# Kernel tuning notes

Measured on AMD Instinct MI355X. Metric: run time of the kernel, lower is better.

The kernel has to match this reference:

```python
import jax, jax.numpy as jnp
import numpy as np

B = 2_000_000
OVERLAP_WEIGHT = 0.5
EPS = 1e-6


def setup_inputs() -> dict:
    key = jax.random.key(0)
    k1, k2 = jax.random.split(key)
    preds = jax.random.normal(k1, (B, 10), dtype=jnp.float32)
    targets = jax.random.normal(k2, (B, 10), dtype=jnp.float32)
    return {"preds": preds, "targets": targets}


def _quat_to_rot(q):
    # q: (B,4) in xyzw order, assumed normalized. Returns (B,3,3),
    # matching the (transposed-convention) matrix in the torch source.
    x, y, z, w = q[:, 0], q[:, 1], q[:, 2], q[:, 3]
    r = jnp.stack([
        1 - 2 * y * y - 2 * z * z, 2 * x * y + 2 * z * w, 2 * x * z - 2 * y * w,
        2 * x * y - 2 * z * w, 1 - 2 * x * x - 2 * z * z, 2 * y * z + 2 * x * w,
        2 * x * z + 2 * y * w, 2 * y * z - 2 * x * w, 1 - 2 * x * x - 2 * y * y,
    ], axis=-1)
    return r.reshape(-1, 3, 3)


def _overlaps(pred_params, gt_params):
    pred_c, pred_d, pred_q = pred_params[:, :3], pred_params[:, 3:6], pred_params[:, 6:]
    gt_c, gt_d, gt_q = gt_params[:, :3], gt_params[:, 3:6], gt_params[:, 6:]
    pred_q = pred_q / jnp.linalg.norm(pred_q, axis=-1, keepdims=True)
    gt_q = gt_q / jnp.linalg.norm(gt_q, axis=-1, keepdims=True)
    pred_rot = _quat_to_rot(pred_q)  # (B,3,3)
    gt_rot = _quat_to_rot(gt_q)      # (B,3,3)
    # trace(pred_rot.T @ gt_rot) = sum of elementwise products
    rot_align = jnp.clip(jnp.sum(pred_rot * gt_rot, axis=(1, 2)) / 3.0, 0.0, 1.0)
    pred_ext = jnp.abs(jnp.einsum('bij,bj->bi', pred_rot, pred_d / 2))
    gt_ext = jnp.abs(jnp.einsum('bij,bj->bi', gt_rot, gt_d / 2))
    center_diff = jnp.abs(pred_c - gt_c)
    overlap_per_axis = jnp.maximum(jnp.minimum(pred_ext, gt_ext) * 2 - center_diff, 0.0) \
        / (pred_ext + gt_ext + EPS)
    overlap = jnp.prod(overlap_per_axis, axis=-1) * rot_align
    return jnp.clip(overlap, 0.0, 1.0)


def _smooth_l1(preds, targets):
    d = preds - targets
    ad = jnp.abs(d)
    return jnp.mean(jnp.where(ad < 1.0, 0.5 * d * d, ad - 0.5))


def reference(preds, targets):
    param_loss = _smooth_l1(preds, targets)
    overlap = _overlaps(preds, targets)
    return param_loss + OVERLAP_WEIGHT * (1.0 - jnp.mean(overlap))
```

## Files before the change

kernel.cpp:

```cpp
#include <hip/hip_runtime.h>


#define B_ROWS 2000000
#define THREADS 256
#define CHUNK_ROWS 256
#define F4_SIDE 640
#define N_CHUNKS 7813
#define GRID 1024
constexpr float OVERLAP_WEIGHT = 0.5f;
constexpr float EPS_F = 1e-6f;
constexpr int TOTAL_F4 = 5000000;

__device__ __forceinline__ void gload_lds16(const float4* g, float4* l) {
    __builtin_amdgcn_global_load_lds(
        (const __attribute__((address_space(1))) void*)g,
        (__attribute__((address_space(3))) void*)l, 16, 0, 0);
}

__device__ __forceinline__ void quat_to_rot(float x, float y, float z, float w,
                                            float R[9]) {
    R[0] = 1.f - 2.f*y*y - 2.f*z*z;
    R[1] = 2.f*x*y + 2.f*z*w;
    R[2] = 2.f*x*z - 2.f*y*w;
    R[3] = 2.f*x*y - 2.f*z*w;
    R[4] = 1.f - 2.f*x*x - 2.f*z*z;
    R[5] = 2.f*y*z + 2.f*x*w;
    R[6] = 2.f*x*z + 2.f*y*w;
    R[7] = 2.f*y*z - 2.f*x*w;
    R[8] = 1.f - 2.f*x*x - 2.f*y*y;
}

__global__ __launch_bounds__(THREADS) void hybrid_loss_main(
    const float4* __restrict__ preds4, const float4* __restrict__ targets4,
    float* __restrict__ acc)
{
    __shared__ __align__(16) float4 lds[2][2][F4_SIDE];

    const int tid  = threadIdx.x;
    const int wave = tid >> 6;
    const int lane = tid & 63;

    float psum = 0.f, osum = 0.f;

    auto stage = [&](int buf, int c) {
        const int gb = c * F4_SIDE;
        for (int r = wave; r < 10; r += 4) {
            int idx = gb + r * 64 + lane;
            if (idx >= TOTAL_F4) idx = TOTAL_F4 - 1;
            gload_lds16(preds4   + idx, &lds[buf][0][r * 64]);
            gload_lds16(targets4 + idx, &lds[buf][1][r * 64]);
        }
    };

    int c = blockIdx.x;
    int cur = 0;
    stage(0, c);
    __syncthreads();

    while (true) {
        const int cn = c + GRID;
        const bool more = (cn < N_CHUNKS);
        if (more) stage(cur ^ 1, cn);

        if (c * CHUNK_ROWS + tid < B_ROWS) {
            float p[10], t[10];
            const float2* lp = reinterpret_cast<const float2*>(
                reinterpret_cast<const float*>(&lds[cur][0][0]) + tid * 10);
            const float2* lt = reinterpret_cast<const float2*>(
                reinterpret_cast<const float*>(&lds[cur][1][0]) + tid * 10);
            #pragma unroll
            for (int i = 0; i < 5; ++i) {
                float2 a = lp[i]; p[2*i] = a.x; p[2*i+1] = a.y;
                float2 b = lt[i]; t[2*i] = b.x; t[2*i+1] = b.y;
            }

            #pragma unroll
            for (int i = 0; i < 10; ++i) {
                float d  = p[i] - t[i];
                float ad = fabsf(d);
                psum += (ad < 1.f) ? 0.5f * d * d : ad - 0.5f;
            }

            float pqn = sqrtf(p[6]*p[6] + p[7]*p[7] + p[8]*p[8] + p[9]*p[9]);
            float tqn = sqrtf(t[6]*t[6] + t[7]*t[7] + t[8]*t[8] + t[9]*t[9]);
            float pri = 1.f / pqn, tri = 1.f / tqn;
            float PR[9], TR[9];
            quat_to_rot(p[6]*pri, p[7]*pri, p[8]*pri, p[9]*pri, PR);
            quat_to_rot(t[6]*tri, t[7]*tri, t[8]*tri, t[9]*tri, TR);

            float ra = 0.f;
            #pragma unroll
            for (int i = 0; i < 9; ++i) ra += PR[i] * TR[i];
            ra = fminf(fmaxf(ra * (1.f/3.f), 0.f), 1.f);

            float ov = ra;
            #pragma unroll
            for (int i = 0; i < 3; ++i) {
                float pe = fabsf(PR[3*i+0]*(p[3]*0.5f) + PR[3*i+1]*(p[4]*0.5f) + PR[3*i+2]*(p[5]*0.5f));
                float te = fabsf(TR[3*i+0]*(t[3]*0.5f) + TR[3*i+1]*(t[4]*0.5f) + TR[3*i+2]*(t[5]*0.5f));
                float cd = fabsf(p[i] - t[i]);
                float ax = fmaxf(fminf(pe, te) * 2.f - cd, 0.f) / (pe + te + EPS_F);
                ov *= ax;
            }
            ov = fminf(fmaxf(ov, 0.f), 1.f);
            osum += ov;
        }

        __syncthreads();
        if (!more) break;
        c = cn;
        cur ^= 1;
    }

    #pragma unroll
    for (int off = 32; off > 0; off >>= 1) {
        psum += __shfl_down(psum, off);
        osum += __shfl_down(osum, off);
    }
    float* red = reinterpret_cast<float*>(&lds[0][0][0]);
    if (lane == 0) { red[wave] = psum; red[4 + wave] = osum; }
    __syncthreads();
    if (tid == 0) {
        float P = red[0] + red[1] + red[2] + red[3];
        float O = red[4] + red[5] + red[6] + red[7];
        atomicAdd(&acc[0], P);
        atomicAdd(&acc[1], O);
    }
}

__global__ void hybrid_loss_finalize(const float* __restrict__ acc,
                                     float* __restrict__ out) {
    out[0] = acc[0] * (1.f / (10.f * (float)B_ROWS))
           + OVERLAP_WEIGHT * (1.f - acc[1] * (1.f / (float)B_ROWS));
}

extern "C" void kernel_launch(void* const* d_in, const int* in_sizes, int n_in,
                              void* d_out, int out_size, void* d_ws, size_t ws_size,
                              hipStream_t stream) {
    const float4* preds4   = (const float4*)d_in[0];
    const float4* targets4 = (const float4*)d_in[1];
    float* out = (float*)d_out;
    float* acc = (float*)d_ws;

    hipMemsetAsync(acc, 0, 2 * sizeof(float), stream);

    hybrid_loss_main<<<GRID, THREADS, 0, stream>>>(preds4, targets4, acc);
    hybrid_loss_finalize<<<1, 1, 0, stream>>>(acc, out);
}
```

Measured before the change: 191.2 us.

## Halve block size, split preds/targets loads per wave, unroll double-buffer loop

```diff
diff --git a/kernel.cpp b/kernel.cpp
--- a/kernel.cpp
+++ b/kernel.cpp
@@ -2,14 +2,13 @@
 
 
 #define B_ROWS 2000000
-#define THREADS 256
-#define CHUNK_ROWS 256
-#define F4_SIDE 640
-#define N_CHUNKS 7813
-#define GRID 1024
+#define THREADS 128
+#define CHUNK_ROWS 128
+#define F4_SIDE 320
+#define N_CHUNKS 15625
+#define GRID 2048
 constexpr float OVERLAP_WEIGHT = 0.5f;
 constexpr float EPS_F = 1e-6f;
-constexpr int TOTAL_F4 = 5000000;
 
 __device__ __forceinline__ void gload_lds16(const float4* g, float4* l) {
     __builtin_amdgcn_global_load_lds(
@@ -30,11 +29,12 @@
     R[8] = 1.f - 2.f*x*x - 2.f*y*y;
 }
 
-__global__ __launch_bounds__(THREADS) void hybrid_loss_main(
+__global__ __launch_bounds__(THREADS, 4) void hybrid_loss_main(
     const float4* __restrict__ preds4, const float4* __restrict__ targets4,
     float* __restrict__ acc)
 {
-    __shared__ __align__(16) float4 lds[2][2][F4_SIDE];
+    __shared__ __align__(16) float4 P0[F4_SIDE], T0[F4_SIDE];
+    __shared__ __align__(16) float4 P1[F4_SIDE], T1[F4_SIDE];
 
     const int tid  = threadIdx.x;
     const int wave = tid >> 6;
@@ -42,74 +42,80 @@
 
     float psum = 0.f, osum = 0.f;
 
-    auto stage = [&](int buf, int c) {
-        const int gb = c * F4_SIDE;
-        for (int r = wave; r < 10; r += 4) {
-            int idx = gb + r * 64 + lane;
-            if (idx >= TOTAL_F4) idx = TOTAL_F4 - 1;
-            gload_lds16(preds4   + idx, &lds[buf][0][r * 64]);
-            gload_lds16(targets4 + idx, &lds[buf][1][r * 64]);
+    auto stage = [&](float4* LP, float4* LT, int c) {
+        const int gb = c * F4_SIDE + lane;
+        if (wave == 0) {
+            #pragma unroll
+            for (int r = 0; r < 5; ++r)
+                gload_lds16(preds4 + gb + r * 64, LP + r * 64);
+        } else {
+            #pragma unroll
+            for (int r = 0; r < 5; ++r)
+                gload_lds16(targets4 + gb + r * 64, LT + r * 64);
         }
     };
 
-    int c = blockIdx.x;
-    int cur = 0;
-    stage(0, c);
-    __syncthreads();
-
-    while (true) {
-        const int cn = c + GRID;
-        const bool more = (cn < N_CHUNKS);
-        if (more) stage(cur ^ 1, cn);
-
-        if (c * CHUNK_ROWS + tid < B_ROWS) {
-            float p[10], t[10];
-            const float2* lp = reinterpret_cast<const float2*>(
-                reinterpret_cast<const float*>(&lds[cur][0][0]) + tid * 10);
-            const float2* lt = reinterpret_cast<const float2*>(
-                reinterpret_cast<const float*>(&lds[cur][1][0]) + tid * 10);
-            #pragma unroll
-            for (int i = 0; i < 5; ++i) {
-                float2 a = lp[i]; p[2*i] = a.x; p[2*i+1] = a.y;
-                float2 b = lt[i]; t[2*i] = b.x; t[2*i+1] = b.y;
-            }
-
-            #pragma unroll
-            for (int i = 0; i < 10; ++i) {
-                float d  = p[i] - t[i];
-                float ad = fabsf(d);
-                psum += (ad < 1.f) ? 0.5f * d * d : ad - 0.5f;
-            }
-
-            float pqn = sqrtf(p[6]*p[6] + p[7]*p[7] + p[8]*p[8] + p[9]*p[9]);
-            float tqn = sqrtf(t[6]*t[6] + t[7]*t[7] + t[8]*t[8] + t[9]*t[9]);
-            float pri = 1.f / pqn, tri = 1.f / tqn;
-            float PR[9], TR[9];
-            quat_to_rot(p[6]*pri, p[7]*pri, p[8]*pri, p[9]*pri, PR);
-            quat_to_rot(t[6]*tri, t[7]*tri, t[8]*tri, t[9]*tri, TR);
-
-            float ra = 0.f;
-            #pragma unroll
-            for (int i = 0; i < 9; ++i) ra += PR[i] * TR[i];
-            ra = fminf(fmaxf(ra * (1.f/3.f), 0.f), 1.f);
-
-            float ov = ra;
-            #pragma unroll
-            for (int i = 0; i < 3; ++i) {
-                float pe = fabsf(PR[3*i+0]*(p[3]*0.5f) + PR[3*i+1]*(p[4]*0.5f) + PR[3*i+2]*(p[5]*0.5f));
-                float te = fabsf(TR[3*i+0]*(t[3]*0.5f) + TR[3*i+1]*(t[4]*0.5f) + TR[3*i+2]*(t[5]*0.5f));
-                float cd = fabsf(p[i] - t[i]);
-                float ax = fmaxf(fminf(pe, te) * 2.f - cd, 0.f) / (pe + te + EPS_F);
-                ov *= ax;
-            }
-            ov = fminf(fmaxf(ov, 0.f), 1.f);
-            osum += ov;
+    auto compute = [&](const float4* LP, const float4* LT) {
+        float p[10], t[10];
+        const float2* lp = reinterpret_cast<const float2*>(
+            reinterpret_cast<const float*>(LP) + tid * 10);
+        const float2* lt = reinterpret_cast<const float2*>(
+            reinterpret_cast<const float*>(LT) + tid * 10);
+        #pragma unroll
+        for (int i = 0; i < 5; ++i) {
+            float2 a = lp[i]; p[2*i] = a.x; p[2*i+1] = a.y;
+            float2 b = lt[i]; t[2*i] = b.x; t[2*i+1] = b.y;
         }
 
+        #pragma unroll
+        for (int i = 0; i < 10; ++i) {
+            float d  = p[i] - t[i];
+            float ad = fabsf(d);
+            psum += (ad < 1.f) ? 0.5f * d * d : ad - 0.5f;
+        }
+
+        float pqn = sqrtf(p[6]*p[6] + p[7]*p[7] + p[8]*p[8] + p[9]*p[9]);
+        float tqn = sqrtf(t[6]*t[6] + t[7]*t[7] + t[8]*t[8] + t[9]*t[9]);
+        float pri = 1.f / pqn, tri = 1.f / tqn;
+        float PR[9], TR[9];
+        quat_to_rot(p[6]*pri, p[7]*pri, p[8]*pri, p[9]*pri, PR);
+        quat_to_rot(t[6]*tri, t[7]*tri, t[8]*tri, t[9]*tri, TR);
+
+        float ra = 0.f;
+        #pragma unroll
+        for (int i = 0; i < 9; ++i) ra += PR[i] * TR[i];
+        ra = fminf(fmaxf(ra * (1.f/3.f), 0.f), 1.f);
+
+        float ov = ra;
+        #pragma unroll
+        for (int i = 0; i < 3; ++i) {
+            float pe = fabsf(PR[3*i+0]*(p[3]*0.5f) + PR[3*i+1]*(p[4]*0.5f) + PR[3*i+2]*(p[5]*0.5f));
+            float te = fabsf(TR[3*i+0]*(t[3]*0.5f) + TR[3*i+1]*(t[4]*0.5f) + TR[3*i+2]*(t[5]*0.5f));
+            float cd = fabsf(p[i] - t[i]);
+            float ax = fmaxf(fminf(pe, te) * 2.f - cd, 0.f) / (pe + te + EPS_F);
+            ov *= ax;
+        }
+        ov = fminf(fmaxf(ov, 0.f), 1.f);
+        osum += ov;
+    };
+
+    int c0 = blockIdx.x;
+    stage(P0, T0, c0);
+    __syncthreads();
+    int c1 = c0 + GRID;
+
+    for (;;) {
+        if (c1 < N_CHUNKS) stage(P1, T1, c1);
+        compute(P0, T0);
         __syncthreads();
-        if (!more) break;
-        c = cn;
-        cur ^= 1;
+        if (c1 >= N_CHUNKS) break;
+        c0 = c1 + GRID;
+
+        if (c0 < N_CHUNKS) stage(P0, T0, c0);
+        compute(P1, T1);
+        __syncthreads();
+        if (c0 >= N_CHUNKS) break;
+        c1 = c0 + GRID;
     }
 
     #pragma unroll
@@ -117,14 +123,12 @@
         psum += __shfl_down(psum, off);
         osum += __shfl_down(osum, off);
     }
-    float* red = reinterpret_cast<float*>(&lds[0][0][0]);
-    if (lane == 0) { red[wave] = psum; red[4 + wave] = osum; }
+    float* red = reinterpret_cast<float*>(P0);
+    if (lane == 0) { red[wave] = psum; red[2 + wave] = osum; }
     __syncthreads();
     if (tid == 0) {
-        float P = red[0] + red[1] + red[2] + red[3];
-        float O = red[4] + red[5] + red[6] + red[7];
-        atomicAdd(&acc[0], P);
-        atomicAdd(&acc[1], O);
+        atomicAdd(&acc[0], red[0] + red[1]);
+        atomicAdd(&acc[1], red[2] + red[3]);
     }
 }
 
```

After: 213.1 us. +11.4%, slower.

## Replace direct global-to-LDS loads with register-staged double buffering

Applied to the files above, without the earlier changes.

```diff
diff --git a/kernel.cpp b/kernel.cpp
--- a/kernel.cpp
+++ b/kernel.cpp
@@ -10,12 +10,6 @@
 constexpr float OVERLAP_WEIGHT = 0.5f;
 constexpr float EPS_F = 1e-6f;
 constexpr int TOTAL_F4 = 5000000;
-
-__device__ __forceinline__ void gload_lds16(const float4* g, float4* l) {
-    __builtin_amdgcn_global_load_lds(
-        (const __attribute__((address_space(1))) void*)g,
-        (__attribute__((address_space(3))) void*)l, 16, 0, 0);
-}
 
 __device__ __forceinline__ void quat_to_rot(float x, float y, float z, float w,
                                             float R[9]) {
@@ -30,44 +24,46 @@
     R[8] = 1.f - 2.f*x*x - 2.f*y*y;
 }
 
-__global__ __launch_bounds__(THREADS) void hybrid_loss_main(
+__global__ __launch_bounds__(THREADS, 4) void hybrid_loss_main(
     const float4* __restrict__ preds4, const float4* __restrict__ targets4,
     float* __restrict__ acc)
 {
-    __shared__ __align__(16) float4 lds[2][2][F4_SIDE];
+    __shared__ __align__(16) float4 P0[F4_SIDE], T0[F4_SIDE];
+    __shared__ __align__(16) float4 P1[F4_SIDE], T1[F4_SIDE];
 
     const int tid  = threadIdx.x;
     const int wave = tid >> 6;
     const int lane = tid & 63;
+    const bool lo  = (tid < 128);
 
     float psum = 0.f, osum = 0.f;
 
-    auto stage = [&](int buf, int c) {
+    float4 a0, a1, a2, b0, b1, b2;
+
+    auto LD = [&](int c) {
         const int gb = c * F4_SIDE;
-        for (int r = wave; r < 10; r += 4) {
-            int idx = gb + r * 64 + lane;
-            if (idx >= TOTAL_F4) idx = TOTAL_F4 - 1;
-            gload_lds16(preds4   + idx, &lds[buf][0][r * 64]);
-            gload_lds16(targets4 + idx, &lds[buf][1][r * 64]);
+        int i0 = gb + tid;        if (i0 >= TOTAL_F4) i0 = TOTAL_F4 - 1;
+        int i1 = gb + 256 + tid;  if (i1 >= TOTAL_F4) i1 = TOTAL_F4 - 1;
+        a0 = preds4[i0];   a1 = preds4[i1];
+        b0 = targets4[i0]; b1 = targets4[i1];
+        if (lo) {
+            int i2 = gb + 512 + tid; if (i2 >= TOTAL_F4) i2 = TOTAL_F4 - 1;
+            a2 = preds4[i2]; b2 = targets4[i2];
         }
     };
+    auto WR = [&](float4* P, float4* T) {
+        P[tid] = a0;       P[256 + tid] = a1;
+        T[tid] = b0;       T[256 + tid] = b1;
+        if (lo) { P[512 + tid] = a2; T[512 + tid] = b2; }
+    };
 
-    int c = blockIdx.x;
-    int cur = 0;
-    stage(0, c);
-    __syncthreads();
-
-    while (true) {
-        const int cn = c + GRID;
-        const bool more = (cn < N_CHUNKS);
-        if (more) stage(cur ^ 1, cn);
-
+    auto compute = [&](const float4* LP4, const float4* LT4, int c) {
         if (c * CHUNK_ROWS + tid < B_ROWS) {
             float p[10], t[10];
             const float2* lp = reinterpret_cast<const float2*>(
-                reinterpret_cast<const float*>(&lds[cur][0][0]) + tid * 10);
+                reinterpret_cast<const float*>(LP4) + tid * 10);
             const float2* lt = reinterpret_cast<const float2*>(
-                reinterpret_cast<const float*>(&lds[cur][1][0]) + tid * 10);
+                reinterpret_cast<const float*>(LT4) + tid * 10);
             #pragma unroll
             for (int i = 0; i < 5; ++i) {
                 float2 a = lp[i]; p[2*i] = a.x; p[2*i+1] = a.y;
@@ -105,11 +101,31 @@
             ov = fminf(fmaxf(ov, 0.f), 1.f);
             osum += ov;
         }
+    };
 
+    int cc = blockIdx.x;
+    LD(cc);
+    WR(P0, T0);
+    __syncthreads();
+
+    for (;;) {
+        int cn = cc + GRID;
+        bool more = (cn < N_CHUNKS);
+        if (more) LD(cn);
+        compute(P0, T0, cc);
+        if (more) WR(P1, T1);
         __syncthreads();
         if (!more) break;
-        c = cn;
-        cur ^= 1;
+        cc = cn;
+
+        cn = cc + GRID;
+        more = (cn < N_CHUNKS);
+        if (more) LD(cn);
+        compute(P1, T1, cc);
+        if (more) WR(P0, T0);
+        __syncthreads();
+        if (!more) break;
+        cc = cn;
     }
 
     #pragma unroll
@@ -117,14 +133,13 @@
         psum += __shfl_down(psum, off);
         osum += __shfl_down(osum, off);
     }
-    float* red = reinterpret_cast<float*>(&lds[0][0][0]);
+    __syncthreads();
+    float* red = reinterpret_cast<float*>(P0);
     if (lane == 0) { red[wave] = psum; red[4 + wave] = osum; }
     __syncthreads();
     if (tid == 0) {
-        float P = red[0] + red[1] + red[2] + red[3];
-        float O = red[4] + red[5] + red[6] + red[7];
-        atomicAdd(&acc[0], P);
-        atomicAdd(&acc[1], O);
+        atomicAdd(&acc[0], red[0] + red[1] + red[2] + red[3]);
+        atomicAdd(&acc[1], red[4] + red[5] + red[6] + red[7]);
     }
 }
 
```

After: 190.6 us. About the same (-0.3%).
